# Kernel tuning notes

Measured on AMD Instinct MI355X. Metric: run time of the kernel, lower is better.

## Reference

```python
import jax, jax.numpy as jnp
import numpy as np

HIDDEN = 1024
NUM_HEADS = 16
HEAD_DIM = HIDDEN // NUM_HEADS


def setup_inputs() -> dict:
    key = jax.random.key(0)
    ks = jax.random.split(key, 11)
    s = 1.0 / np.sqrt(HIDDEN)
    x = jax.random.normal(ks[0], (4, 2048, HIDDEN), dtype=jnp.float32)
    Wq = jax.random.uniform(ks[1], (HIDDEN, HIDDEN), jnp.float32, -s, s)
    bq = jax.random.uniform(ks[2], (HIDDEN,), jnp.float32, -s, s)
    Wk = jax.random.uniform(ks[3], (HIDDEN, HIDDEN), jnp.float32, -s, s)
    bk = jax.random.uniform(ks[4], (HIDDEN,), jnp.float32, -s, s)
    Wv = jax.random.uniform(ks[5], (HIDDEN, HIDDEN), jnp.float32, -s, s)
    bv = jax.random.uniform(ks[6], (HIDDEN,), jnp.float32, -s, s)
    Wo = jax.random.uniform(ks[7], (HIDDEN, HIDDEN), jnp.float32, -s, s)
    bo = jax.random.uniform(ks[8], (HIDDEN,), jnp.float32, -s, s)
    ln_g = jnp.ones((HIDDEN,), jnp.float32)
    ln_b = jnp.zeros((HIDDEN,), jnp.float32)
    return {"x": x, "Wq": Wq, "bq": bq, "Wk": Wk, "bk": bk,
            "Wv": Wv, "bv": bv, "Wo": Wo, "bo": bo,
            "ln_g": ln_g, "ln_b": ln_b}


def _layer_norm(x, g, b, eps=1e-5):
    mu = jnp.mean(x, axis=-1, keepdims=True)
    var = jnp.var(x, axis=-1, keepdims=True)
    return (x - mu) * jax.lax.rsqrt(var + eps) * g + b


def reference(x, Wq, bq, Wk, bk, Wv, bv, Wo, bo, ln_g, ln_b):
    B, S, _ = x.shape
    residual = x
    h = _layer_norm(x, ln_g, ln_b)
    # projections (torch Linear: y = h @ W.T + b)
    q = (h @ Wq.T + bq).reshape(B, S, NUM_HEADS, HEAD_DIM).transpose(0, 2, 1, 3)
    k = (h @ Wk.T + bk).reshape(B, S, NUM_HEADS, HEAD_DIM).transpose(0, 2, 1, 3)
    v = (h @ Wv.T + bv).reshape(B, S, NUM_HEADS, HEAD_DIM).transpose(0, 2, 1, 3)
    scores = jnp.einsum('bhqd,bhkd->bhqk', q, k) / np.sqrt(HEAD_DIM).astype(np.float32)
    weights = jax.nn.softmax(scores, axis=-1)  # dropout = identity (eval mode)
    context = jnp.einsum('bhqk,bhkd->bhqd', weights, v)
    context = context.transpose(0, 2, 1, 3).reshape(B, S, HIDDEN)
    out = context @ Wo.T + bo
    return out + residual
```

## Files before the change

kernel.cpp:

```cpp
#include <hip/hip_runtime.h>

typedef unsigned short u16;
typedef unsigned int   u32;
using bf16x8 = __attribute__((ext_vector_type(8))) __bf16;
using f32x4  = __attribute__((ext_vector_type(4))) float;
using u32x2  = __attribute__((ext_vector_type(2))) unsigned int;

__device__ __forceinline__ u16 f2b(float f){
  union { float f; u32 i; } v; v.f = f;
  u32 r = v.i + 0x7FFFu + ((v.i >> 16) & 1u);
  return (u16)(r >> 16);
}
__device__ __forceinline__ u32 pk_bf16_trunc(float a, float b){
  return __builtin_amdgcn_perm(__float_as_uint(b), __float_as_uint(a), 0x07060302u);
}

__global__ __launch_bounds__(256) void cvt_w(const float* __restrict__ s0, const float* __restrict__ s1,
                                             const float* __restrict__ s2, const float* __restrict__ s3,
                                             u16* __restrict__ d){
  const float* srcs[4] = {s0, s1, s2, s3};
  const float* s = srcs[blockIdx.y];
  u16* dd = d + (size_t)blockIdx.y * (1024u * 1024u);
  const int i = (blockIdx.x * 256 + threadIdx.x) * 4;
  float4 v = *(const float4*)(s + i);
  uint2 o;
  o.x = (u32)f2b(v.x) | ((u32)f2b(v.y) << 16);
  o.y = (u32)f2b(v.z) | ((u32)f2b(v.w) << 16);
  *(uint2*)(dd + i) = o;
}

__global__ __launch_bounds__(256) void ln_kernel(const float* __restrict__ x, const float* __restrict__ g,
                                                 const float* __restrict__ be, u16* __restrict__ h){
  const int row = blockIdx.x, tid = threadIdx.x;
  const float* xr = x + (size_t)row * 1024u;
  float4 raw = *(const float4*)(xr + tid * 4);
  float s  = raw.x + raw.y + raw.z + raw.w;
  float sq = raw.x*raw.x + raw.y*raw.y + raw.z*raw.z + raw.w*raw.w;
  #pragma unroll
  for (int m = 1; m < 64; m <<= 1){ s += __shfl_xor(s, m); sq += __shfl_xor(sq, m); }
  __shared__ float ws[4], wq[4];
  if ((tid & 63) == 0){ ws[tid >> 6] = s; wq[tid >> 6] = sq; }
  __syncthreads();
  s  = ws[0] + ws[1] + ws[2] + ws[3];
  sq = wq[0] + wq[1] + wq[2] + wq[3];
  const float mu = s * (1.0f / 1024.0f);
  const float rstd = rsqrtf(sq * (1.0f / 1024.0f) - mu * mu + 1e-5f);
  float4 gg = *(const float4*)(g + tid * 4);
  float4 bb = *(const float4*)(be + tid * 4);
  float y0 = (raw.x - mu) * rstd * gg.x + bb.x;
  float y1 = (raw.y - mu) * rstd * gg.y + bb.y;
  float y2 = (raw.z - mu) * rstd * gg.z + bb.z;
  float y3 = (raw.w - mu) * rstd * gg.w + bb.w;
  uint2 outv;
  outv.x = (u32)f2b(y0) | ((u32)f2b(y1) << 16);
  outv.y = (u32)f2b(y2) | ((u32)f2b(y3) << 16);
  *(uint2*)(h + (size_t)row * 1024u + tid * 4) = outv;
}

__global__ __launch_bounds__(256) void gemm_qkv(const u16* __restrict__ A, const u16* __restrict__ Wcat,
                                                const float* __restrict__ bq, const float* __restrict__ bk,
                                                const float* __restrict__ bv,
                                                u16* __restrict__ qo, u16* __restrict__ ko, u16* __restrict__ vt){
  __shared__ u16 lA[128 * 32];
  __shared__ u16 lB[128 * 32];
  const int tid = threadIdx.x;
  const int lane = tid & 63, wv = tid >> 6, l15 = lane & 15, quad = lane >> 4;
  const int wr = wv >> 1, wc = wv & 1;
  const int row0 = blockIdx.x * 128, col0 = blockIdx.y * 128;
  const int K = 1024;
  f32x4 acc[4][4] = {};
  for (int kt = 0; kt < 32; ++kt){
    __syncthreads();
    #pragma unroll
    for (int jj = 0; jj < 2; ++jj){
      int idx = jj * 256 + tid;
      int r = idx >> 2, c = idx & 3;
      __builtin_amdgcn_global_load_lds(
        (const __attribute__((address_space(1))) void*)(A + (size_t)(row0 + r) * K + (kt * 32 + c * 8)),
        (__attribute__((address_space(3))) void*)(&lA[idx * 8]), 16, 0, 0);
      __builtin_amdgcn_global_load_lds(
        (const __attribute__((address_space(1))) void*)(Wcat + (size_t)(col0 + r) * K + (kt * 32 + c * 8)),
        (__attribute__((address_space(3))) void*)(&lB[idx * 8]), 16, 0, 0);
    }
    __syncthreads();
    bf16x8 af[4], bf[4];
    #pragma unroll
    for (int i = 0; i < 4; ++i) af[i] = *(const bf16x8*)&lA[(wr * 64 + i * 16 + l15) * 32 + quad * 8];
    #pragma unroll
    for (int j = 0; j < 4; ++j) bf[j] = *(const bf16x8*)&lB[(wc * 64 + j * 16 + l15) * 32 + quad * 8];
    #pragma unroll
    for (int i = 0; i < 4; ++i)
      #pragma unroll
      for (int j = 0; j < 4; ++j)
        acc[i][j] = __builtin_amdgcn_mfma_f32_16x16x32_bf16(af[i], bf[j], acc[i][j], 0, 0, 0);
  }
  const int sel = col0 >> 10;
  if (sel < 2){
    const float* bias = (sel == 0) ? bq : bk;
    u16* dst = (sel == 0) ? qo : ko;
    #pragma unroll
    for (int i = 0; i < 4; ++i){
      const int grow = row0 + wr * 64 + i * 16 + quad * 4;
      #pragma unroll
      for (int j = 0; j < 4; ++j){
        const int gcol = (col0 & 1023) + wc * 64 + j * 16 + l15;
        const float bb = bias[gcol];
        #pragma unroll
        for (int r = 0; r < 4; ++r){
          size_t off = (size_t)(grow + r) * 1024u + gcol;
          dst[off] = f2b(acc[i][j][r] + bb);
        }
      }
    }
  } else {
    #pragma unroll
    for (int i = 0; i < 4; ++i){
      const int grow = row0 + wr * 64 + i * 16 + quad * 4;
      const int bb_  = grow >> 11, srem = grow & 2047;
      #pragma unroll
      for (int j = 0; j < 4; ++j){
        const int gcol = (col0 & 1023) + wc * 64 + j * 16 + l15;
        const int head = gcol >> 6, d = gcol & 63;
        const float bv_ = bv[gcol];
        uint2 pk;
        pk.x = (u32)f2b(acc[i][j][0] + bv_) | ((u32)f2b(acc[i][j][1] + bv_) << 16);
        pk.y = (u32)f2b(acc[i][j][2] + bv_) | ((u32)f2b(acc[i][j][3] + bv_) << 16);
        *(uint2*)(vt + ((size_t)((bb_ * 16 + head) * 64 + d)) * 2048u + srem) = pk;
      }
    }
  }
}

__global__ __launch_bounds__(256) void gemm_out(const u16* __restrict__ A, const u16* __restrict__ W,
                                                const float* __restrict__ bias, const float* __restrict__ res,
                                                float* __restrict__ C, int M, int N, int K){
  __shared__ u16 lA[128 * 32];
  __shared__ u16 lB[128 * 32];
  const int tid = threadIdx.x;
  const int lane = tid & 63, wv = tid >> 6, l15 = lane & 15, quad = lane >> 4;
  const int wr = wv >> 1, wc = wv & 1;
  const int row0 = blockIdx.x * 128, col0 = blockIdx.y * 128;
  f32x4 acc[4][4] = {};
  const int nkt = K >> 5;
  for (int kt = 0; kt < nkt; ++kt){
    __syncthreads();
    #pragma unroll
    for (int jj = 0; jj < 2; ++jj){
      int idx = jj * 256 + tid;
      int r = idx >> 2, c = idx & 3;
      __builtin_amdgcn_global_load_lds(
        (const __attribute__((address_space(1))) void*)(A + (size_t)(row0 + r) * K + (kt * 32 + c * 8)),
        (__attribute__((address_space(3))) void*)(&lA[idx * 8]), 16, 0, 0);
      __builtin_amdgcn_global_load_lds(
        (const __attribute__((address_space(1))) void*)(W + (size_t)(col0 + r) * K + (kt * 32 + c * 8)),
        (__attribute__((address_space(3))) void*)(&lB[idx * 8]), 16, 0, 0);
    }
    __syncthreads();
    bf16x8 af[4], bf[4];
    #pragma unroll
    for (int i = 0; i < 4; ++i) af[i] = *(const bf16x8*)&lA[(wr * 64 + i * 16 + l15) * 32 + quad * 8];
    #pragma unroll
    for (int j = 0; j < 4; ++j) bf[j] = *(const bf16x8*)&lB[(wc * 64 + j * 16 + l15) * 32 + quad * 8];
    #pragma unroll
    for (int i = 0; i < 4; ++i)
      #pragma unroll
      for (int j = 0; j < 4; ++j)
        acc[i][j] = __builtin_amdgcn_mfma_f32_16x16x32_bf16(af[i], bf[j], acc[i][j], 0, 0, 0);
  }
  #pragma unroll
  for (int i = 0; i < 4; ++i){
    const int grow = row0 + wr * 64 + i * 16 + quad * 4;
    #pragma unroll
    for (int j = 0; j < 4; ++j){
      const int gcol = col0 + wc * 64 + j * 16 + l15;
      const float bb = bias[gcol];
      #pragma unroll
      for (int r = 0; r < 4; ++r){
        size_t off = (size_t)(grow + r) * N + gcol;
        C[off] = acc[i][j][r] + bb + res[off];
      }
    }
  }
}

__global__ __launch_bounds__(256, 2) void attn_kernel(const u16* __restrict__ Q, const u16* __restrict__ K,
                                                      const u16* __restrict__ Vt, u16* __restrict__ O){
  __shared__ u16 kls[2][64 * 64];
  __shared__ u16 vls[2][64 * 64];
  const int tid = threadIdx.x;
  const int lane = tid & 63, wv = tid >> 6, l15 = lane & 15, quad = lane >> 4;
  const int bh = blockIdx.x & 63, qt = blockIdx.x >> 6;
  const int b = bh >> 4, hh = bh & 15;
  const int q0 = qt * 256;
  const u16* Qg = Q + ((size_t)b * 2048u) * 1024u + hh * 64;
  const u16* Kg = K + ((size_t)b * 2048u) * 1024u + hh * 64;
  const u16* Vg = Vt + (size_t)bh * 64u * 2048u;
  u16* Og = O + ((size_t)b * 2048u) * 1024u + hh * 64;

  const int sr = tid >> 3, sc = tid & 7, sr2 = sr + 32;
  const int sx = (sc ^ (sr & 7)) * 8;
  const int c0 = ((quad ^ (l15 & 7))) * 8;

  const float QSCALE = 0.125f * 1.44269504f;
  bf16x8 qf2[4][2];
  #pragma unroll
  for (int g = 0; g < 4; ++g)
    #pragma unroll
    for (int kk = 0; kk < 2; ++kk){
      qf2[g][kk] = *(const bf16x8*)(Qg + (size_t)(q0 + wv * 64 + g * 16 + l15) * 1024u + kk * 32 + quad * 8);
      #pragma unroll
      for (int e = 0; e < 8; ++e) qf2[g][kk][e] = (__bf16)((float)qf2[g][kk][e] * QSCALE);
    }

  bf16x8 ones_f;
  {
    const __bf16 onev = (__bf16)1.0f, zerov = (__bf16)0.0f;
    #pragma unroll
    for (int e = 0; e < 8; ++e) ones_f[e] = (l15 == 0) ? onev : zerov;
  }

  f32x4 o2[4][4] = {};
  f32x4 o_l[4] = {};
  const f32x4 zf = {0.f, 0.f, 0.f, 0.f};

  uint4 kr0, kr1, vr0, vr1;
  kr0 = *(const uint4*)(Kg + (size_t)sr  * 1024u + sc * 8);
  vr0 = *(const uint4*)(Vg + (size_t)sr  * 2048u + sc * 8);
  kr1 = *(const uint4*)(Kg + (size_t)sr2 * 1024u + sc * 8);
  vr1 = *(const uint4*)(Vg + (size_t)sr2 * 2048u + sc * 8);
  *(uint4*)&kls[0][sr  * 64 + sx] = kr0;
  *(uint4*)&vls[0][sr  * 64 + sx] = vr0;
  *(uint4*)&kls[0][sr2 * 64 + sx] = kr1;
  *(uint4*)&vls[0][sr2 * 64 + sx] = vr1;
  kr0 = *(const uint4*)(Kg + (size_t)(64 + sr)  * 1024u + sc * 8);
  vr0 = *(const uint4*)(Vg + (size_t)sr  * 2048u + 64 + sc * 8);
  kr1 = *(const uint4*)(Kg + (size_t)(64 + sr2) * 1024u + sc * 8);
  vr1 = *(const uint4*)(Vg + (size_t)sr2 * 2048u + 64 + sc * 8);
  __syncthreads();

  for (int kt = 0; kt < 32; ++kt){
    const int cur = kt & 1;
    const u16* kb = kls[cur];
    const u16* vb = vls[cur];
    if (kt < 31){
      u16* kw = kls[cur ^ 1];
      u16* vw = vls[cur ^ 1];
      *(uint4*)&kw[sr  * 64 + sx] = kr0;
      *(uint4*)&vw[sr  * 64 + sx] = vr0;
      *(uint4*)&kw[sr2 * 64 + sx] = kr1;
      *(uint4*)&vw[sr2 * 64 + sx] = vr1;
    }
    if (kt < 30){
      const int s0 = (kt + 2) * 64;
      kr0 = *(const uint4*)(Kg + (size_t)(s0 + sr)  * 1024u + sc * 8);
      vr0 = *(const uint4*)(Vg + (size_t)sr  * 2048u + s0 + sc * 8);
      kr1 = *(const uint4*)(Kg + (size_t)(s0 + sr2) * 1024u + sc * 8);
      vr1 = *(const uint4*)(Vg + (size_t)sr2 * 2048u + s0 + sc * 8);
    }

    f32x4 s2[4][4];
    #pragma unroll
    for (int j = 0; j < 4; ++j){
      const int rb = (j * 16 + l15) * 64;
      bf16x8 kfr0 = *(const bf16x8*)&kb[rb + c0];
      bf16x8 kfr1 = *(const bf16x8*)&kb[rb + (c0 ^ 32)];
      #pragma unroll
      for (int g = 0; g < 4; ++g){
        f32x4 a = __builtin_amdgcn_mfma_f32_16x16x32_bf16(kfr0, qf2[g][0], zf, 0, 0, 0);
        s2[g][j] = __builtin_amdgcn_mfma_f32_16x16x32_bf16(kfr1, qf2[g][1], a, 0, 0, 0);
      }
    }

    #pragma unroll
    for (int g = 0; g < 4; ++g)
      #pragma unroll
      for (int j = 0; j < 4; ++j)
        #pragma unroll
        for (int r = 0; r < 4; ++r)
          s2[g][j][r] = __builtin_amdgcn_exp2f(s2[g][j][r]);

    #pragma unroll
    for (int kk = 0; kk < 2; ++kk){
      bf16x8 afr[4];
      #pragma unroll
      for (int g = 0; g < 4; ++g){
        const int j0 = kk * 2, j1 = j0 + 1;
        u32 A0 = pk_bf16_trunc(s2[g][j0][0], s2[g][j0][1]);
        u32 A1 = pk_bf16_trunc(s2[g][j0][2], s2[g][j0][3]);
        u32 B0 = pk_bf16_trunc(s2[g][j1][0], s2[g][j1][1]);
        u32 B1 = pk_bf16_trunc(s2[g][j1][2], s2[g][j1][3]);
        u32x2 r1 = __builtin_amdgcn_permlane32_swap(A0, B0, false, false);
        u32x2 r2 = __builtin_amdgcn_permlane16_swap(r1[0], r1[1], false, false);
        u32x2 r3 = __builtin_amdgcn_permlane32_swap(A1, B1, false, false);
        u32x2 r4 = __builtin_amdgcn_permlane16_swap(r3[0], r3[1], false, false);
        union { uint4 u; bf16x8 v; } cv;
        cv.u.x = r2[0]; cv.u.y = r4[0]; cv.u.z = r2[1]; cv.u.w = r4[1];
        afr[g] = cv.v;
      }
      #pragma unroll
      for (int g = 0; g < 4; ++g)
        o_l[g] = __builtin_amdgcn_mfma_f32_16x16x32_bf16(afr[g], ones_f, o_l[g], 0, 0, 0);
      #pragma unroll
      for (int j2 = 0; j2 < 4; ++j2){
        bf16x8 bfr = *(const bf16x8*)&vb[(j2 * 16 + l15) * 64 + (c0 ^ (kk * 32))];
        #pragma unroll
        for (int g = 0; g < 4; ++g)
          o2[g][j2] = __builtin_amdgcn_mfma_f32_16x16x32_bf16(afr[g], bfr, o2[g][j2], 0, 0, 0);
      }
    }
    __syncthreads();
  }

  #pragma unroll
  for (int g = 0; g < 4; ++g){
    float lr[4];
    #pragma unroll
    for (int r = 0; r < 4; ++r) lr[r] = 1.0f / __shfl(o_l[g][r], quad * 16);
    #pragma unroll
    for (int j2 = 0; j2 < 4; ++j2){
      #pragma unroll
      for (int r = 0; r < 4; ++r){
        const int qrow = q0 + wv * 64 + g * 16 + quad * 4 + r;
        const int d = j2 * 16 + l15;
        Og[(size_t)qrow * 1024u + d] = f2b(o2[g][j2][r] * lr[r]);
      }
    }
  }
}

extern "C" void kernel_launch(void* const* d_in, const int* in_sizes, int n_in,
                              void* d_out, int out_size, void* d_ws, size_t ws_size,
                              hipStream_t stream){
  (void)in_sizes; (void)n_in; (void)out_size; (void)ws_size;
  const float* x   = (const float*)d_in[0];
  const float* Wq  = (const float*)d_in[1];
  const float* bq  = (const float*)d_in[2];
  const float* Wk  = (const float*)d_in[3];
  const float* bk  = (const float*)d_in[4];
  const float* Wv  = (const float*)d_in[5];
  const float* bv  = (const float*)d_in[6];
  const float* Wo  = (const float*)d_in[7];
  const float* bo  = (const float*)d_in[8];
  const float* lng = (const float*)d_in[9];
  const float* lnb = (const float*)d_in[10];
  float* out = (float*)d_out;

  const size_t TE = (size_t)8192 * 1024;
  u16* ws0 = (u16*)d_ws;
  u16* ws1 = ws0 + TE;
  u16* ws2 = ws1 + TE;
  u16* wsw = ws2 + TE;
  u16* wob = wsw + (size_t)3 * 1024 * 1024;
  u16* vt  = (u16*)d_out;

  cvt_w<<<dim3(1024, 4), 256, 0, stream>>>(Wq, Wk, Wv, Wo, wsw);
  ln_kernel<<<dim3(8192), 256, 0, stream>>>(x, lng, lnb, ws0);
  gemm_qkv<<<dim3(64, 24), 256, 0, stream>>>(ws0, wsw, bq, bk, bv, ws1, ws2, vt);
  attn_kernel<<<dim3(512), 256, 0, stream>>>(ws1, ws2, vt, ws1);
  gemm_out<<<dim3(64, 8), 256, 0, stream>>>(ws1, wob, bo, x, out, 8192, 1024, 1024);
}
```

Measured before the change: 279.3 us.

## Swizzle GEMM LDS tiles and stage V-transpose store through LDS

Applies an XOR swizzle to the 16-byte chunk column of the global-to-LDS staging in both the QKV and output GEMMs. Fragment reads then hit different LDS banks and no longer conflict. It also rewrites the V-transposed epilogue of the QKV GEMM to transpose each wave's tile through LDS, so the global writes become contiguous 16-byte stores along the sequence instead of scattered 8-byte stores. In exchange the epilogue gains an extra LDS round trip and barrier, and the source pointers are precomputed outside the k-loop.

After: 275.4 us. About the same (-1.4%).

```diff
diff --git a/kernel.cpp b/kernel.cpp
--- a/kernel.cpp
+++ b/kernel.cpp
@@ -61,33 +61,44 @@
                                                 const float* __restrict__ bq, const float* __restrict__ bk,
                                                 const float* __restrict__ bv,
                                                 u16* __restrict__ qo, u16* __restrict__ ko, u16* __restrict__ vt){
-  __shared__ u16 lA[128 * 32];
-  __shared__ u16 lB[128 * 32];
+  __shared__ u16 lds[8192];
+  u16* lA = lds;
+  u16* lB = lds + 4096;
   const int tid = threadIdx.x;
   const int lane = tid & 63, wv = tid >> 6, l15 = lane & 15, quad = lane >> 4;
   const int wr = wv >> 1, wc = wv & 1;
   const int row0 = blockIdx.x * 128, col0 = blockIdx.y * 128;
   const int K = 1024;
+
+  const int r0_ = tid >> 2,         c0_ = tid & 3;
+  const int r1_ = (256 + tid) >> 2, c1_ = (256 + tid) & 3;
+  const u16* Asrc0 = A    + (size_t)(row0 + r0_) * K + (c0_ ^ ((r0_ >> 1) & 3)) * 8;
+  const u16* Asrc1 = A    + (size_t)(row0 + r1_) * K + (c1_ ^ ((r1_ >> 1) & 3)) * 8;
+  const u16* Bsrc0 = Wcat + (size_t)(col0 + r0_) * K + (c0_ ^ ((r0_ >> 1) & 3)) * 8;
+  const u16* Bsrc1 = Wcat + (size_t)(col0 + r1_) * K + (c1_ ^ ((r1_ >> 1) & 3)) * 8;
+  const int cr = (quad ^ ((l15 >> 1) & 3)) * 8;
+
   f32x4 acc[4][4] = {};
   for (int kt = 0; kt < 32; ++kt){
     __syncthreads();
-    #pragma unroll
-    for (int jj = 0; jj < 2; ++jj){
-      int idx = jj * 256 + tid;
-      int r = idx >> 2, c = idx & 3;
-      __builtin_amdgcn_global_load_lds(
-        (const __attribute__((address_space(1))) void*)(A + (size_t)(row0 + r) * K + (kt * 32 + c * 8)),
-        (__attribute__((address_space(3))) void*)(&lA[idx * 8]), 16, 0, 0);
-      __builtin_amdgcn_global_load_lds(
-        (const __attribute__((address_space(1))) void*)(Wcat + (size_t)(col0 + r) * K + (kt * 32 + c * 8)),
-        (__attribute__((address_space(3))) void*)(&lB[idx * 8]), 16, 0, 0);
-    }
+    __builtin_amdgcn_global_load_lds(
+      (const __attribute__((address_space(1))) void*)(Asrc0 + kt * 32),
+      (__attribute__((address_space(3))) void*)(&lA[tid * 8]), 16, 0, 0);
+    __builtin_amdgcn_global_load_lds(
+      (const __attribute__((address_space(1))) void*)(Asrc1 + kt * 32),
+      (__attribute__((address_space(3))) void*)(&lA[(256 + tid) * 8]), 16, 0, 0);
+    __builtin_amdgcn_global_load_lds(
+      (const __attribute__((address_space(1))) void*)(Bsrc0 + kt * 32),
+      (__attribute__((address_space(3))) void*)(&lB[tid * 8]), 16, 0, 0);
+    __builtin_amdgcn_global_load_lds(
+      (const __attribute__((address_space(1))) void*)(Bsrc1 + kt * 32),
+      (__attribute__((address_space(3))) void*)(&lB[(256 + tid) * 8]), 16, 0, 0);
     __syncthreads();
     bf16x8 af[4], bf[4];
     #pragma unroll
-    for (int i = 0; i < 4; ++i) af[i] = *(const bf16x8*)&lA[(wr * 64 + i * 16 + l15) * 32 + quad * 8];
-    #pragma unroll
-    for (int j = 0; j < 4; ++j) bf[j] = *(const bf16x8*)&lB[(wc * 64 + j * 16 + l15) * 32 + quad * 8];
+    for (int i = 0; i < 4; ++i) af[i] = *(const bf16x8*)&lA[(wr * 64 + i * 16 + l15) * 32 + cr];
+    #pragma unroll
+    for (int j = 0; j < 4; ++j) bf[j] = *(const bf16x8*)&lB[(wc * 64 + j * 16 + l15) * 32 + cr];
     #pragma unroll
     for (int i = 0; i < 4; ++i)
       #pragma unroll
@@ -113,19 +124,36 @@
       }
     }
   } else {
-    #pragma unroll
-    for (int i = 0; i < 4; ++i){
-      const int grow = row0 + wr * 64 + i * 16 + quad * 4;
-      const int bb_  = grow >> 11, srem = grow & 2047;
-      #pragma unroll
-      for (int j = 0; j < 4; ++j){
-        const int gcol = (col0 & 1023) + wc * 64 + j * 16 + l15;
-        const int head = gcol >> 6, d = gcol & 63;
-        const float bv_ = bv[gcol];
-        uint2 pk;
-        pk.x = (u32)f2b(acc[i][j][0] + bv_) | ((u32)f2b(acc[i][j][1] + bv_) << 16);
-        pk.y = (u32)f2b(acc[i][j][2] + bv_) | ((u32)f2b(acc[i][j][3] + bv_) << 16);
-        *(uint2*)(vt + ((size_t)((bb_ * 16 + head) * 64 + d)) * 2048u + srem) = pk;
+    __syncthreads();
+    u16* pw = lds + wv * 2048;
+    const int bglob = row0 >> 11;
+    const int head  = ((col0 & 1023) >> 6) + wc;
+    const int srem0 = (row0 & 2047) + wr * 64;
+    const size_t vbase = (size_t)((bglob * 16 + head) * 64) * 2048u;
+    #pragma unroll
+    for (int p = 0; p < 2; ++p){
+      #pragma unroll
+      for (int i2 = 0; i2 < 2; ++i2){
+        const int i = p * 2 + i2;
+        #pragma unroll
+        for (int j = 0; j < 4; ++j){
+          const int d = j * 16 + l15;
+          const float bv_ = bv[(col0 & 1023) + wc * 64 + d];
+          const int u = (i2 * 4 + quad) ^ (d & 7);
+          uint2 pk;
+          pk.x = (u32)f2b(acc[i][j][0] + bv_) | ((u32)f2b(acc[i][j][1] + bv_) << 16);
+          pk.y = (u32)f2b(acc[i][j][2] + bv_) | ((u32)f2b(acc[i][j][3] + bv_) << 16);
+          *(uint2*)&pw[d * 32 + u * 4] = pk;
+        }
+      }
+      const int dl = lane;
+      #pragma unroll
+      for (int c = 0; c < 4; ++c){
+        const int u0 = (2 * c) ^ (dl & 7), u1 = (2 * c + 1) ^ (dl & 7);
+        uint2 lo = *(const uint2*)&pw[dl * 32 + u0 * 4];
+        uint2 hi = *(const uint2*)&pw[dl * 32 + u1 * 4];
+        uint4 o4; o4.x = lo.x; o4.y = lo.y; o4.z = hi.x; o4.w = hi.y;
+        *(uint4*)(vt + vbase + (size_t)dl * 2048u + srem0 + p * 32 + c * 8) = o4;
       }
     }
   }
@@ -140,27 +168,37 @@
   const int lane = tid & 63, wv = tid >> 6, l15 = lane & 15, quad = lane >> 4;
   const int wr = wv >> 1, wc = wv & 1;
   const int row0 = blockIdx.x * 128, col0 = blockIdx.y * 128;
+
+  const int r0_ = tid >> 2,         c0_ = tid & 3;
+  const int r1_ = (256 + tid) >> 2, c1_ = (256 + tid) & 3;
+  const u16* Asrc0 = A + (size_t)(row0 + r0_) * K + (c0_ ^ ((r0_ >> 1) & 3)) * 8;
+  const u16* Asrc1 = A + (size_t)(row0 + r1_) * K + (c1_ ^ ((r1_ >> 1) & 3)) * 8;
+  const u16* Bsrc0 = W + (size_t)(col0 + r0_) * K + (c0_ ^ ((r0_ >> 1) & 3)) * 8;
+  const u16* Bsrc1 = W + (size_t)(col0 + r1_) * K + (c1_ ^ ((r1_ >> 1) & 3)) * 8;
+  const int cr = (quad ^ ((l15 >> 1) & 3)) * 8;
+
   f32x4 acc[4][4] = {};
   const int nkt = K >> 5;
   for (int kt = 0; kt < nkt; ++kt){
     __syncthreads();
-    #pragma unroll
-    for (int jj = 0; jj < 2; ++jj){
-      int idx = jj * 256 + tid;
-      int r = idx >> 2, c = idx & 3;
-      __builtin_amdgcn_global_load_lds(
-        (const __attribute__((address_space(1))) void*)(A + (size_t)(row0 + r) * K + (kt * 32 + c * 8)),
-        (__attribute__((address_space(3))) void*)(&lA[idx * 8]), 16, 0, 0);
-      __builtin_amdgcn_global_load_lds(
-        (const __attribute__((address_space(1))) void*)(W + (size_t)(col0 + r) * K + (kt * 32 + c * 8)),
-        (__attribute__((address_space(3))) void*)(&lB[idx * 8]), 16, 0, 0);
-    }
+    __builtin_amdgcn_global_load_lds(
+      (const __attribute__((address_space(1))) void*)(Asrc0 + kt * 32),
+      (__attribute__((address_space(3))) void*)(&lA[tid * 8]), 16, 0, 0);
+    __builtin_amdgcn_global_load_lds(
+      (const __attribute__((address_space(1))) void*)(Asrc1 + kt * 32),
+      (__attribute__((address_space(3))) void*)(&lA[(256 + tid) * 8]), 16, 0, 0);
+    __builtin_amdgcn_global_load_lds(
+      (const __attribute__((address_space(1))) void*)(Bsrc0 + kt * 32),
+      (__attribute__((address_space(3))) void*)(&lB[tid * 8]), 16, 0, 0);
+    __builtin_amdgcn_global_load_lds(
+      (const __attribute__((address_space(1))) void*)(Bsrc1 + kt * 32),
+      (__attribute__((address_space(3))) void*)(&lB[(256 + tid) * 8]), 16, 0, 0);
     __syncthreads();
     bf16x8 af[4], bf[4];
     #pragma unroll
-    for (int i = 0; i < 4; ++i) af[i] = *(const bf16x8*)&lA[(wr * 64 + i * 16 + l15) * 32 + quad * 8];
-    #pragma unroll
-    for (int j = 0; j < 4; ++j) bf[j] = *(const bf16x8*)&lB[(wc * 64 + j * 16 + l15) * 32 + quad * 8];
+    for (int i = 0; i < 4; ++i) af[i] = *(const bf16x8*)&lA[(wr * 64 + i * 16 + l15) * 32 + cr];
+    #pragma unroll
+    for (int j = 0; j < 4; ++j) bf[j] = *(const bf16x8*)&lB[(wc * 64 + j * 16 + l15) * 32 + cr];
     #pragma unroll
     for (int i = 0; i < 4; ++i)
       #pragma unroll
```
